# Performance work log

Hardware: AMD Instinct MI355X
Metric: run time of the kernel (lower is better)

## Reference

```python
import jax, jax.numpy as jnp
import numpy as np

NUM_HEAD = 16
D_Q = 512
D_KV = 512
ROPE_BASE = 10000.0


def _cos_sin(seq_len, dim):
    # Replicates calculate_cos_sin: theta = base**(-2*ids) / (dim//2)
    pos = jnp.arange(seq_len, dtype=jnp.float32)[:, None]          # (S,1)
    ids = jnp.arange(dim // 2, dtype=jnp.float32)                  # (D/2,)
    theta = (ROPE_BASE ** (-2.0 * ids)) / (dim // 2)
    r = pos * theta[None, :]                                       # (S, D/2)
    return jnp.cos(r), jnp.sin(r)


def _rope(x, cos, sin):
    b, s, d = x.shape
    xv = x.reshape(b, s, d // 2, 2)
    x0, x1 = xv[..., 0], xv[..., 1]
    out = jnp.stack([x0 * cos - x1 * sin, x1 * cos + x0 * sin], axis=-1)
    return out.reshape(b, s, d)


def setup_inputs() -> dict:
    key = jax.random.key(0)
    ks = jax.random.split(key, 10)
    d_model, d_q, d_kv = 1024, D_Q, D_KV
    b, s = 2, 2048
    w = lambda k, i, o: jax.random.normal(k, (i, o), dtype=jnp.float32) * 0.02
    return {
        "x": jax.random.normal(ks[0], (b, s, d_model), dtype=jnp.float32),
        "Wd_q_w": w(ks[1], d_model, d_q), "Wd_q_b": jnp.zeros((d_q,), jnp.float32),
        "Wu_q_w": w(ks[2], d_q, d_model), "Wu_q_b": jnp.zeros((d_model,), jnp.float32),
        "Wq_r_w": w(ks[3], d_q, d_model), "Wq_r_b": jnp.zeros((d_model,), jnp.float32),
        "Wk_r_w": w(ks[4], d_model, d_model), "Wk_r_b": jnp.zeros((d_model,), jnp.float32),
        "Wd_kv_w": w(ks[5], d_model, d_kv), "Wd_kv_b": jnp.zeros((d_kv,), jnp.float32),
        "Wu_k_w": w(ks[6], d_kv, d_model), "Wu_k_b": jnp.zeros((d_model,), jnp.float32),
        "Wu_v_w": w(ks[7], d_kv, d_model), "Wu_v_b": jnp.zeros((d_model,), jnp.float32),
        "Wo_w": w(ks[8], d_model, d_model), "Wo_b": jnp.zeros((d_model,), jnp.float32),
    }


def reference(x, Wd_q_w, Wd_q_b, Wu_q_w, Wu_q_b, Wq_r_w, Wq_r_b,
              Wk_r_w, Wk_r_b, Wd_kv_w, Wd_kv_b, Wu_k_w, Wu_k_b,
              Wu_v_w, Wu_v_b, Wo_w, Wo_b):
    b, s, d_model = x.shape
    h = NUM_HEAD
    hd = d_model // h
    scale = jnp.sqrt(jnp.float32(h + D_KV + D_Q))

    def heads(t):  # (b,s,d) -> (b,h,s,hd)
        return t.reshape(b, s, h, hd).transpose(0, 2, 1, 3)

    cos, sin = _cos_sin(s, d_model)

    ct_q = x @ Wd_q_w + Wd_q_b                                   # (b,s,d_q)
    qt_c = heads(ct_q @ Wu_q_w + Wu_q_b)
    qt_r = heads(_rope(ct_q @ Wq_r_w + Wq_r_b, cos, sin))
    query = qt_c + qt_r                                          # (b,h,s,hd)

    ct_kv = x @ Wd_kv_w + Wd_kv_b                                # (b,s,d_kv)
    kt_c = heads(ct_kv @ Wu_k_w + Wu_k_b)
    kt_r = heads(_rope(x @ Wk_r_w + Wk_r_b, cos, sin))
    key = kt_c + kt_r
    value = heads(ct_kv @ Wu_v_w + Wu_v_b)

    attn = jnp.einsum('bhqd,bhkd->bhqk', query, key) / scale
    attn = jax.nn.softmax(attn, axis=-1)
    out = jnp.einsum('bhqk,bhkd->bhqd', attn, value)
    out = out.transpose(0, 2, 1, 3).reshape(b, s, d_model)
    return out @ Wo_w + Wo_b
```

## Files before the change

kernel.cpp:

```cpp
#include <hip/hip_runtime.h>
#include <hip/hip_bf16.h>
#include <math.h>
#include <limits.h>

typedef __hip_bfloat16 bf16;
typedef __bf16 bf16x8 __attribute__((ext_vector_type(8)));
typedef float  f32x4  __attribute__((ext_vector_type(4)));

#define DEVI __device__ __forceinline__

static constexpr int Bb     = 2;
static constexpr int Ss     = 2048;
static constexpr int DMODEL = 1024;
static constexpr int NTOK   = Bb * Ss;

DEVI float bf2f(bf16 v) { return __bfloat162float(v); }
DEVI bf16  f2bf(float v) { return __float2bfloat16(v); }

DEVI unsigned int packbf(float lo, float hi) {
  union { bf16 b; unsigned short u; } a, c;
  a.b = f2bf(lo); c.b = f2bf(hi);
  return ((unsigned int)c.u << 16) | a.u;
}
DEVI float bfu2f(unsigned short u) {
  unsigned int x = (unsigned int)u << 16;
  float f; __builtin_memcpy(&f, &x, 4); return f;
}

DEVI void async_load16(const bf16* g, bf16* l) {
  __builtin_amdgcn_global_load_lds((const __attribute__((address_space(1))) void*)g,
                                   (__attribute__((address_space(3))) void*)l, 16, 0, 0);
}

__global__ __launch_bounds__(256) void convert_kernel(
    const float* __restrict__ in, bf16* __restrict__ out, int n4) {
  const int t = blockIdx.x * blockDim.x + threadIdx.x;
  if (t >= n4) return;
  const float4 v = ((const float4*)in)[t];
  uint2 o; o.x = packbf(v.x, v.y); o.y = packbf(v.z, v.w);
  *(uint2*)&out[(size_t)t * 4] = o;
}

struct TransDesc { const float* src; bf16* dst; int R; int C; int tstart; };
struct TransPack { TransDesc d[8]; };

__global__ __launch_bounds__(256) void transpose8_kernel(TransPack p) {
  const int t = blockIdx.x;
  int i = 0;
#pragma unroll
  for (int j = 1; j < 8; ++j) if (t >= p.d[j].tstart) i = j;
  const float* __restrict__ in = p.d[i].src;
  bf16* __restrict__ out = p.d[i].dst;
  const int R = p.d[i].R, C = p.d[i].C;
  const int rel = t - p.d[i].tstart;
  const int tilesC = C >> 6;
  const int r0 = (rel / tilesC) * 64, c0 = (rel % tilesC) * 64;

  __shared__ bf16 tl[64][65];
  const int tc = threadIdx.x & 63, tr = threadIdx.x >> 6;
#pragma unroll
  for (int q = 0; q < 16; ++q) {
    int r = tr + q * 4;
    tl[r][tc] = f2bf(in[(size_t)(r0 + r) * C + c0 + tc]);
  }
  __syncthreads();
#pragma unroll
  for (int q = 0; q < 16; ++q) {
    int r = tr + q * 4;
    out[(size_t)(c0 + r) * R + r0 + tc] = tl[tc][r];
  }
}

struct GemmDesc {
  const bf16* A; const bf16* WT; const float* b1; const float* b2; bf16* C;
  int lda, ldb, ldc, K, bsplit, nTX, blkStart, biasRow;
};
struct GemmBatch { GemmDesc d[4]; };

__global__ __launch_bounds__(256) void gemm_batch_kernel(GemmBatch gb) {
  const int t = blockIdx.x;
  int di = 0;
#pragma unroll
  for (int j = 1; j < 4; ++j) if (t >= gb.d[j].blkStart) di = j;
  const GemmDesc D = gb.d[di];
  const int rel = t - D.blkStart;
  const int tileN = (rel % D.nTX) * 128;
  const int tileM = (rel / D.nTX) * 128;

  __shared__ bf16 ldsA[128 * 32];
  __shared__ bf16 ldsB[128 * 32];
  const int tid = threadIdx.x;
  const int lane = tid & 63;
  const int w = tid >> 6;
  const int wr = w >> 1, wc = w & 1;
  const int l15 = lane & 15, lg = lane >> 4;
  const int lrow = lane >> 2;
  const int lcol = (lane & 3) * 8;

  f32x4 acc[4][4] = {};

  for (int k0 = 0; k0 < D.K; k0 += 32) {
    async_load16(D.A  + (size_t)(tileM + w * 32 +      lrow) * D.lda + k0 + lcol, &ldsA[(w * 32) * 32]);
    async_load16(D.A  + (size_t)(tileM + w * 32 + 16 + lrow) * D.lda + k0 + lcol, &ldsA[(w * 32 + 16) * 32]);
    async_load16(D.WT + (size_t)(tileN + w * 32 +      lrow) * D.ldb + k0 + lcol, &ldsB[(w * 32) * 32]);
    async_load16(D.WT + (size_t)(tileN + w * 32 + 16 + lrow) * D.ldb + k0 + lcol, &ldsB[(w * 32 + 16) * 32]);
    __syncthreads();

    bf16x8 af[4], bfr[4];
#pragma unroll
    for (int i = 0; i < 4; ++i) {
      af[i]  = *(const bf16x8*)&ldsA[(wr * 64 + i * 16 + l15) * 32 + lg * 8];
      bfr[i] = *(const bf16x8*)&ldsB[(wc * 64 + i * 16 + l15) * 32 + lg * 8];
    }
#pragma unroll
    for (int i = 0; i < 4; ++i)
#pragma unroll
      for (int j = 0; j < 4; ++j)
        acc[i][j] = __builtin_amdgcn_mfma_f32_16x16x32_bf16(af[i], bfr[j], acc[i][j], 0, 0, 0);
    __syncthreads();
  }

  const int mbase = tileM + wr * 64;
  const int nbase = tileN + wc * 64;
#pragma unroll
  for (int j = 0; j < 4; ++j) {
    int col = nbase + j * 16 + l15;
    float bvc = D.biasRow ? 0.0f : (col < D.bsplit ? D.b1[col] : D.b2[col - D.bsplit]);
#pragma unroll
    for (int i = 0; i < 4; ++i)
#pragma unroll
      for (int r = 0; r < 4; ++r) {
        int row = mbase + i * 16 + lg * 4 + r;
        float bv = D.biasRow ? D.b1[row] : bvc;
        D.C[(size_t)row * D.ldc + col] = f2bf(acc[i][j][r] + bv);
      }
  }
}

__global__ __launch_bounds__(256) void gemm_kernel_f32(
    const bf16* __restrict__ A, int lda,
    const bf16* __restrict__ WT, int ldb,
    const float* __restrict__ b1,
    float* __restrict__ Cout, int ldc, int K) {
  __shared__ bf16 ldsA[128 * 32];
  __shared__ bf16 ldsB[128 * 32];
  const int tid = threadIdx.x;
  const int lane = tid & 63;
  const int w = tid >> 6;
  const int wr = w >> 1, wc = w & 1;
  const int tileM = blockIdx.y * 128;
  const int tileN = blockIdx.x * 128;
  const int l15 = lane & 15, lg = lane >> 4;
  const int lrow = lane >> 2;
  const int lcol = (lane & 3) * 8;

  f32x4 acc[4][4] = {};

  for (int k0 = 0; k0 < K; k0 += 32) {
    async_load16(A  + (size_t)(tileM + w * 32 +      lrow) * lda + k0 + lcol, &ldsA[(w * 32) * 32]);
    async_load16(A  + (size_t)(tileM + w * 32 + 16 + lrow) * lda + k0 + lcol, &ldsA[(w * 32 + 16) * 32]);
    async_load16(WT + (size_t)(tileN + w * 32 +      lrow) * ldb + k0 + lcol, &ldsB[(w * 32) * 32]);
    async_load16(WT + (size_t)(tileN + w * 32 + 16 + lrow) * ldb + k0 + lcol, &ldsB[(w * 32 + 16) * 32]);
    __syncthreads();

    bf16x8 af[4], bfr[4];
#pragma unroll
    for (int i = 0; i < 4; ++i) {
      af[i]  = *(const bf16x8*)&ldsA[(wr * 64 + i * 16 + l15) * 32 + lg * 8];
      bfr[i] = *(const bf16x8*)&ldsB[(wc * 64 + i * 16 + l15) * 32 + lg * 8];
    }
#pragma unroll
    for (int i = 0; i < 4; ++i)
#pragma unroll
      for (int j = 0; j < 4; ++j)
        acc[i][j] = __builtin_amdgcn_mfma_f32_16x16x32_bf16(af[i], bfr[j], acc[i][j], 0, 0, 0);
    __syncthreads();
  }

  const int mbase = tileM + wr * 64;
  const int nbase = tileN + wc * 64;
#pragma unroll
  for (int j = 0; j < 4; ++j) {
    int col = nbase + j * 16 + l15;
    float bvc = b1[col];
#pragma unroll
    for (int i = 0; i < 4; ++i)
#pragma unroll
      for (int r = 0; r < 4; ++r) {
        int row = mbase + i * 16 + lg * 4 + r;
        Cout[(size_t)row * ldc + col] = acc[i][j][r] + bvc;
      }
  }
}

__global__ __launch_bounds__(256) void combine_rope_kernel(
    const bf16* __restrict__ Gc, int ldc_,
    const bf16* __restrict__ Gr, int ldr_,
    bf16* __restrict__ out) {
  const int t = blockIdx.x * blockDim.x + threadIdx.x;
  const int g = t & 127, row = t >> 7;
  const int s = row & (Ss - 1);
  union { bf16x8 v; unsigned short u[8]; } vc, vr;
  vc.v = *(const bf16x8*)&Gc[(size_t)row * ldc_ + (size_t)g * 8];
  vr.v = *(const bf16x8*)&Gr[(size_t)row * ldr_ + (size_t)g * 8];
  uint4 o;
  unsigned int* op = &o.x;
#pragma unroll
  for (int qq = 0; qq < 4; ++qq) {
    const int p = g * 4 + qq;
    float c, sn;
    if (p == 0) {
      float rr = (float)s * (1.0f / 512.0f);
      c = cosf(rr); sn = sinf(rr);
    } else {
      float theta = exp2f(-26.5754247590989f * (float)p) * (1.0f / 512.0f);
      sn = (float)s * theta; c = 1.0f;
    }
    float g0 = bfu2f(vr.u[2 * qq]), g1 = bfu2f(vr.u[2 * qq + 1]);
    float c0 = bfu2f(vc.u[2 * qq]), c1 = bfu2f(vc.u[2 * qq + 1]);
    op[qq] = packbf(c0 + g0 * c - g1 * sn, c1 + g1 * c + g0 * sn);
  }
  *(uint4*)&out[(size_t)row * DMODEL + (size_t)g * 8] = o;
}

__global__ __launch_bounds__(256) void attn_kernel(
    const bf16* __restrict__ Qn, const bf16* __restrict__ Kn,
    const bf16* __restrict__ VT, bf16* __restrict__ AO) {
  const int bh = blockIdx.x, qt = blockIdx.y;
  const int b = bh >> 4, h = bh & 15;
  const int tid = threadIdx.x, lane = tid & 63, w = tid >> 6;
  const int q0 = qt * 64 + w * 16;
  const int l15 = lane & 15, lg = lane >> 4;
  const float SC2 = 0.044736075f;
  const float THR = 11.5415603f;

  __shared__ bf16 ldsK[2][64 * 64];
  __shared__ bf16 ldsV[2][64 * 64];
  __shared__ bf16 ldsP[4][16 * 64];

  const bf16* Kg = Kn + (size_t)(b * Ss) * DMODEL + h * 64;
  const bf16* Vg = VT + (size_t)(h * 64) * NTOK + b * Ss;

  const int r0 = tid >> 3;
  const int srcb = ((tid & 7) * 16) ^ ((r0 & 7) << 4);
  const char* kS0 = (const char*)(Kg + (size_t)r0 * DMODEL) + srcb;
  const char* kS1 = (const char*)(Kg + (size_t)(32 + r0) * DMODEL) + srcb;
  const char* vS0 = (const char*)(Vg + (size_t)r0 * NTOK) + srcb;
  const char* vS1 = (const char*)(Vg + (size_t)(32 + r0) * NTOK) + srcb;
  const ptrdiff_t kAdv = (ptrdiff_t)64 * DMODEL * 2;
  const ptrdiff_t vAdv = 128;

  bf16* kd0_b0 = &ldsK[0][w * 512]; bf16* kd1_b0 = &ldsK[0][2048 + w * 512];
  bf16* kd0_b1 = &ldsK[1][w * 512]; bf16* kd1_b1 = &ldsK[1][2048 + w * 512];
  bf16* vd0_b0 = &ldsV[0][w * 512]; bf16* vd1_b0 = &ldsV[0][2048 + w * 512];
  bf16* vd0_b1 = &ldsV[1][w * 512]; bf16* vd1_b1 = &ldsV[1][2048 + w * 512];

  auto stageTo = [&](bf16* kd0, bf16* kd1, bf16* vd0, bf16* vd1) {
    async_load16((const bf16*)kS0, kd0);
    async_load16((const bf16*)kS1, kd1);
    async_load16((const bf16*)vS0, vd0);
    async_load16((const bf16*)vS1, vd1);
    kS0 += kAdv; kS1 += kAdv; vS0 += vAdv; vS1 += vAdv;
  };

  const int kswz = (l15 & 7) << 4;
  const int xA = (lg * 16) ^ kswz;
  const int xB = (64 + lg * 16) ^ kswz;
  const char* krA0 = (const char*)&ldsK[0][0] + l15 * 128 + xA;
  const char* krB0 = (const char*)&ldsK[0][0] + l15 * 128 + xB;
  const char* krA1 = (const char*)&ldsK[1][0] + l15 * 128 + xA;
  const char* krB1 = (const char*)&ldsK[1][0] + l15 * 128 + xB;
  const char* vrA0 = (const char*)&ldsV[0][0] + l15 * 128 + xA;
  const char* vrB0 = (const char*)&ldsV[0][0] + l15 * 128 + xB;
  const char* vrA1 = (const char*)&ldsV[1][0] + l15 * 128 + xA;
  const char* vrB1 = (const char*)&ldsV[1][0] + l15 * 128 + xB;

  char* Pw = (char*)&ldsP[w][0];
  char* pwr[4];
#pragma unroll
  for (int j = 0; j < 4; ++j) {
    const int chunk = (j * 2 + (lg >> 1)) ^ (l15 & 7);
    pwr[j] = Pw + l15 * 128 + chunk * 16 + (lg & 1) * 8;
  }
  const char* paA = Pw + l15 * 128 + xA;
  const char* paB = Pw + l15 * 128 + xB;

  const bf16* Qbase = Qn + (size_t)(b * Ss + q0 + l15) * DMODEL + h * 64;
  bf16x8 bq0 = *(const bf16x8*)&Qbase[lg * 8];
  bf16x8 bq1 = *(const bf16x8*)&Qbase[32 + lg * 8];

  float m = 0.0f, l = 0.0f;
  f32x4 accO[4] = {};

  auto body = [&](const char* krA, const char* krB, const char* vrA, const char* vrB) {
    f32x4 sa[4] = {};
#pragma unroll
    for (int j = 0; j < 4; ++j) {
      bf16x8 ak0 = *(const bf16x8*)(krA + j * 2048);
      bf16x8 ak1 = *(const bf16x8*)(krB + j * 2048);
      sa[j] = __builtin_amdgcn_mfma_f32_16x16x32_bf16(ak0, bq0, sa[j], 0, 0, 0);
      sa[j] = __builtin_amdgcn_mfma_f32_16x16x32_bf16(ak1, bq1, sa[j], 0, 0, 0);
    }
    float pmaxr = -3.0e38f;
#pragma unroll
    for (int j = 0; j < 4; ++j)
#pragma unroll
      for (int r = 0; r < 4; ++r) pmaxr = fmaxf(pmaxr, sa[j][r]);
    if (__any(fmaf(pmaxr, SC2, -m) > THR)) {
      float px = fmaxf(pmaxr, __shfl_xor(pmaxr, 16, 64));
      px = fmaxf(px, __shfl_xor(px, 32, 64));
      float mnew = fmaxf(m, px * SC2);
      float corr = __builtin_amdgcn_exp2f(m - mnew);
      m = mnew; l *= corr;
      float cr[4];
#pragma unroll
      for (int r = 0; r < 4; ++r) cr[r] = __shfl(corr, lg * 4 + r, 64);
#pragma unroll
      for (int dj = 0; dj < 4; ++dj)
#pragma unroll
        for (int r = 0; r < 4; ++r) accO[dj][r] *= cr[r];
    }
    float p[4][4];
    float ts0 = 0.f, ts1 = 0.f;
#pragma unroll
    for (int j = 0; j < 4; ++j) {
#pragma unroll
      for (int r = 0; r < 4; ++r)
        p[j][r] = __builtin_amdgcn_exp2f(fmaf(sa[j][r], SC2, -m));
      ts0 += p[j][0] + p[j][2];
      ts1 += p[j][1] + p[j][3];
    }
    float ts = ts0 + ts1;
    ts += __shfl_xor(ts, 16, 64);
    ts += __shfl_xor(ts, 32, 64);
    l += ts;
#pragma unroll
    for (int j = 0; j < 4; ++j) {
      uint2 pw;
      pw.x = packbf(p[j][0], p[j][1]);
      pw.y = packbf(p[j][2], p[j][3]);
      *(uint2*)pwr[j] = pw;
    }
    bf16x8 pa0 = *(const bf16x8*)paA;
    bf16x8 pa1 = *(const bf16x8*)paB;
#pragma unroll
    for (int dj = 0; dj < 4; ++dj) {
      bf16x8 bv0 = *(const bf16x8*)(vrA + dj * 2048);
      bf16x8 bv1 = *(const bf16x8*)(vrB + dj * 2048);
      accO[dj] = __builtin_amdgcn_mfma_f32_16x16x32_bf16(pa0, bv0, accO[dj], 0, 0, 0);
      accO[dj] = __builtin_amdgcn_mfma_f32_16x16x32_bf16(pa1, bv1, accO[dj], 0, 0, 0);
    }
  };

  stageTo(kd0_b0, kd1_b0, vd0_b0, vd1_b0);
  for (int tt = 0; tt < 16; ++tt) {
    __syncthreads();
    stageTo(kd0_b1, kd1_b1, vd0_b1, vd1_b1);
    body(krA0, krB0, vrA0, vrB0);
    __syncthreads();
    if (tt < 15) stageTo(kd0_b0, kd1_b0, vd0_b0, vd1_b0);
    body(krA1, krB1, vrA1, vrB1);
  }

  float linv[4];
#pragma unroll
  for (int r = 0; r < 4; ++r) linv[r] = 1.0f / __shfl(l, lg * 4 + r, 64);
#pragma unroll
  for (int dj = 0; dj < 4; ++dj)
#pragma unroll
    for (int r = 0; r < 4; ++r)
      AO[(size_t)(b * Ss + q0 + lg * 4 + r) * DMODEL + h * 64 + dj * 16 + l15] =
          f2bf(accO[dj][r] * linv[r]);
}

extern "C" void kernel_launch(void* const* d_in, const int* in_sizes, int n_in,
                              void* d_out, int out_size, void* d_ws, size_t ws_size,
                              hipStream_t stream) {
  const float* x      = (const float*)d_in[0];
  const float* Wdq    = (const float*)d_in[1];  const float* Wdq_b  = (const float*)d_in[2];
  const float* Wuq    = (const float*)d_in[3];  const float* Wuq_b  = (const float*)d_in[4];
  const float* Wqr    = (const float*)d_in[5];  const float* Wqr_b  = (const float*)d_in[6];
  const float* Wkr    = (const float*)d_in[7];  const float* Wkr_b  = (const float*)d_in[8];
  const float* Wdkv   = (const float*)d_in[9];  const float* Wdkv_b = (const float*)d_in[10];
  const float* Wuk    = (const float*)d_in[11]; const float* Wuk_b  = (const float*)d_in[12];
  const float* Wuv    = (const float*)d_in[13]; const float* Wuv_b  = (const float*)d_in[14];
  const float* Wo     = (const float*)d_in[15]; const float* Wo_b   = (const float*)d_in[16];

  char* ws = (char*)d_ws;
  size_t off = 0;
  bf16* WdqT   = (bf16*)(ws + off); off += (size_t)512  * 1024 * 2;
  bf16* WdkvT  = (bf16*)(ws + off); off += (size_t)512  * 1024 * 2;
  bf16* WuqT   = (bf16*)(ws + off); off += (size_t)1024 * 512  * 2;
  bf16* WqrT   = (bf16*)(ws + off); off += (size_t)1024 * 512  * 2;
  bf16* WukT   = (bf16*)(ws + off); off += (size_t)1024 * 512  * 2;
  bf16* WuvT   = (bf16*)(ws + off); off += (size_t)1024 * 512  * 2;
  bf16* WkrT   = (bf16*)(ws + off); off += (size_t)1024 * 1024 * 2;
  bf16* WoT    = (bf16*)(ws + off); off += (size_t)1024 * 1024 * 2;
  bf16* x_bf   = (bf16*)(ws + off); off += (size_t)NTOK * 1024 * 2;
  bf16* ct     = (bf16*)(ws + off); off += (size_t)NTOK * 1024 * 2;
  bf16* Ga     = (bf16*)(ws + off); off += (size_t)NTOK * 1024 * 2;
  bf16* VTr    = (bf16*)(ws + off); off += (size_t)NTOK * 1024 * 2;
  bf16* Gupk   = x_bf;
  bf16* Qn     = (bf16*)d_out;
  bf16* Kn     = (bf16*)d_out + (size_t)NTOK * DMODEL;
  bf16* AO     = Ga;
  (void)ws_size; (void)in_sizes; (void)n_in; (void)out_size;

  TransPack tp = {{
    { Wdq,  WdqT,  1024, 512,  0    },
    { Wdkv, WdkvT, 1024, 512,  128  },
    { Wuq,  WuqT,  512,  1024, 256  },
    { Wqr,  WqrT,  512,  1024, 384  },
    { Wuk,  WukT,  512,  1024, 512  },
    { Wuv,  WuvT,  512,  1024, 640  },
    { Wkr,  WkrT,  1024, 1024, 768  },
    { Wo,   WoT,   1024, 1024, 1024 },
  }};
  transpose8_kernel<<<1280, 256, 0, stream>>>(tp);
  convert_kernel<<<(NTOK * DMODEL / 4 + 255) / 256, 256, 0, stream>>>(x, x_bf, NTOK * DMODEL / 4);

  GemmBatch ba = {{
    { x_bf, WdqT, Wdq_b, Wdkv_b, ct, 1024, 1024, 1024, 1024, 512,     8, 0,       0 },
    { x_bf, WkrT, Wkr_b, Wkr_b,  Kn, 1024, 1024, 1024, 1024, INT_MAX, 8, 256,     0 },
    { 0, 0, 0, 0, 0, 0, 0, 0, 0, 0, 1, INT_MAX, 0 },
    { 0, 0, 0, 0, 0, 0, 0, 0, 0, 0, 1, INT_MAX, 0 },
  }};
  gemm_batch_kernel<<<512, 256, 0, stream>>>(ba);

  GemmBatch bb = {{
    { ct,       WuqT,     Wuq_b, Wuq_b, Ga,   1024, 512,  1024, 512, INT_MAX, 8,  0,   0 },
    { ct,       WqrT,     Wqr_b, Wqr_b, Qn,   1024, 512,  1024, 512, INT_MAX, 8,  256, 0 },
    { ct + 512, WukT,     Wuk_b, Wuk_b, Gupk, 1024, 512,  1024, 512, INT_MAX, 8,  512, 0 },
    { WuvT,     ct + 512, Wuv_b, Wuv_b, VTr,  512,  1024, NTOK, 512, INT_MAX, 32, 768, 1 },
  }};
  gemm_batch_kernel<<<1024, 256, 0, stream>>>(bb);

  combine_rope_kernel<<<NTOK * 128 / 256, 256, 0, stream>>>(Ga, 1024, Qn, 1024, Qn);
  combine_rope_kernel<<<NTOK * 128 / 256, 256, 0, stream>>>(Gupk, 1024, Kn, 1024, Kn);

  attn_kernel<<<dim3(32, 32), 256, 0, stream>>>(Qn, Kn, VTr, AO);

  gemm_kernel_f32<<<dim3(8, 32), 256, 0, stream>>>(
      AO, 1024, WoT, 1024, Wo_b, (float*)d_out, 1024, 1024);
}
```

Baseline: 197.4 us.

## Fuse weight transpose with input conversion, retile output GEMM, prioritize attention MFMAs

```diff
diff --git a/kernel.cpp b/kernel.cpp
--- a/kernel.cpp
+++ b/kernel.cpp
@@ -32,20 +32,20 @@
                                    (__attribute__((address_space(3))) void*)l, 16, 0, 0);
 }
 
-__global__ __launch_bounds__(256) void convert_kernel(
-    const float* __restrict__ in, bf16* __restrict__ out, int n4) {
-  const int t = blockIdx.x * blockDim.x + threadIdx.x;
-  if (t >= n4) return;
-  const float4 v = ((const float4*)in)[t];
-  uint2 o; o.x = packbf(v.x, v.y); o.y = packbf(v.z, v.w);
-  *(uint2*)&out[(size_t)t * 4] = o;
-}
-
 struct TransDesc { const float* src; bf16* dst; int R; int C; int tstart; };
 struct TransPack { TransDesc d[8]; };
 
-__global__ __launch_bounds__(256) void transpose8_kernel(TransPack p) {
+__global__ __launch_bounds__(256) void trans_conv_kernel(
+    TransPack p, const float* __restrict__ cx, bf16* __restrict__ cxo, int tstartConv) {
+  __shared__ bf16 tl[64][65];
   const int t = blockIdx.x;
+  if (t >= tstartConv) {
+    const int idx = (t - tstartConv) * 256 + threadIdx.x;
+    const float4 v = ((const float4*)cx)[idx];
+    uint2 o; o.x = packbf(v.x, v.y); o.y = packbf(v.z, v.w);
+    *(uint2*)&cxo[(size_t)idx * 4] = o;
+    return;
+  }
   int i = 0;
 #pragma unroll
   for (int j = 1; j < 8; ++j) if (t >= p.d[j].tstart) i = j;
@@ -55,8 +55,6 @@
   const int rel = t - p.d[i].tstart;
   const int tilesC = C >> 6;
   const int r0 = (rel / tilesC) * 64, c0 = (rel % tilesC) * 64;
-
-  __shared__ bf16 tl[64][65];
   const int tc = threadIdx.x & 63, tr = threadIdx.x >> 6;
 #pragma unroll
   for (int q = 0; q < 16; ++q) {
@@ -143,51 +141,48 @@
     const float* __restrict__ b1,
     float* __restrict__ Cout, int ldc, int K) {
   __shared__ bf16 ldsA[128 * 32];
-  __shared__ bf16 ldsB[128 * 32];
+  __shared__ bf16 ldsB[64 * 32];
   const int tid = threadIdx.x;
   const int lane = tid & 63;
   const int w = tid >> 6;
-  const int wr = w >> 1, wc = w & 1;
   const int tileM = blockIdx.y * 128;
-  const int tileN = blockIdx.x * 128;
+  const int tileN = blockIdx.x * 64;
   const int l15 = lane & 15, lg = lane >> 4;
   const int lrow = lane >> 2;
   const int lcol = (lane & 3) * 8;
 
-  f32x4 acc[4][4] = {};
+  f32x4 acc[2][4] = {};
 
   for (int k0 = 0; k0 < K; k0 += 32) {
     async_load16(A  + (size_t)(tileM + w * 32 +      lrow) * lda + k0 + lcol, &ldsA[(w * 32) * 32]);
     async_load16(A  + (size_t)(tileM + w * 32 + 16 + lrow) * lda + k0 + lcol, &ldsA[(w * 32 + 16) * 32]);
-    async_load16(WT + (size_t)(tileN + w * 32 +      lrow) * ldb + k0 + lcol, &ldsB[(w * 32) * 32]);
-    async_load16(WT + (size_t)(tileN + w * 32 + 16 + lrow) * ldb + k0 + lcol, &ldsB[(w * 32 + 16) * 32]);
-    __syncthreads();
-
-    bf16x8 af[4], bfr[4];
-#pragma unroll
-    for (int i = 0; i < 4; ++i) {
-      af[i]  = *(const bf16x8*)&ldsA[(wr * 64 + i * 16 + l15) * 32 + lg * 8];
-      bfr[i] = *(const bf16x8*)&ldsB[(wc * 64 + i * 16 + l15) * 32 + lg * 8];
-    }
-#pragma unroll
-    for (int i = 0; i < 4; ++i)
+    async_load16(WT + (size_t)(tileN + w * 16 + lrow) * ldb + k0 + lcol, &ldsB[(w * 16) * 32]);
+    __syncthreads();
+
+    bf16x8 af[2], bfr[4];
+#pragma unroll
+    for (int i = 0; i < 2; ++i)
+      af[i]  = *(const bf16x8*)&ldsA[(w * 32 + i * 16 + l15) * 32 + lg * 8];
+#pragma unroll
+    for (int j = 0; j < 4; ++j)
+      bfr[j] = *(const bf16x8*)&ldsB[(j * 16 + l15) * 32 + lg * 8];
+#pragma unroll
+    for (int i = 0; i < 2; ++i)
 #pragma unroll
       for (int j = 0; j < 4; ++j)
         acc[i][j] = __builtin_amdgcn_mfma_f32_16x16x32_bf16(af[i], bfr[j], acc[i][j], 0, 0, 0);
     __syncthreads();
   }
 
-  const int mbase = tileM + wr * 64;
-  const int nbase = tileN + wc * 64;
 #pragma unroll
   for (int j = 0; j < 4; ++j) {
-    int col = nbase + j * 16 + l15;
+    int col = tileN + j * 16 + l15;
     float bvc = b1[col];
 #pragma unroll
-    for (int i = 0; i < 4; ++i)
+    for (int i = 0; i < 2; ++i)
 #pragma unroll
       for (int r = 0; r < 4; ++r) {
-        int row = mbase + i * 16 + lg * 4 + r;
+        int row = tileM + w * 32 + i * 16 + lg * 4 + r;
         Cout[(size_t)row * ldc + col] = acc[i][j][r] + bvc;
       }
   }
@@ -294,6 +289,7 @@
 
   auto body = [&](const char* krA, const char* krB, const char* vrA, const char* vrB) {
     f32x4 sa[4] = {};
+    __builtin_amdgcn_s_setprio(1);
 #pragma unroll
     for (int j = 0; j < 4; ++j) {
       bf16x8 ak0 = *(const bf16x8*)(krA + j * 2048);
@@ -301,6 +297,7 @@
       sa[j] = __builtin_amdgcn_mfma_f32_16x16x32_bf16(ak0, bq0, sa[j], 0, 0, 0);
       sa[j] = __builtin_amdgcn_mfma_f32_16x16x32_bf16(ak1, bq1, sa[j], 0, 0, 0);
     }
+    __builtin_amdgcn_s_setprio(0);
     float pmaxr = -3.0e38f;
 #pragma unroll
     for (int j = 0; j < 4; ++j)
@@ -343,6 +340,7 @@
     }
     bf16x8 pa0 = *(const bf16x8*)paA;
     bf16x8 pa1 = *(const bf16x8*)paB;
+    __builtin_amdgcn_s_setprio(1);
 #pragma unroll
     for (int dj = 0; dj < 4; ++dj) {
       bf16x8 bv0 = *(const bf16x8*)(vrA + dj * 2048);
@@ -350,6 +348,7 @@
       accO[dj] = __builtin_amdgcn_mfma_f32_16x16x32_bf16(pa0, bv0, accO[dj], 0, 0, 0);
       accO[dj] = __builtin_amdgcn_mfma_f32_16x16x32_bf16(pa1, bv1, accO[dj], 0, 0, 0);
     }
+    __builtin_amdgcn_s_setprio(0);
   };
 
   stageTo(kd0_b0, kd1_b0, vd0_b0, vd1_b0);
@@ -416,8 +415,7 @@
     { Wkr,  WkrT,  1024, 1024, 768  },
     { Wo,   WoT,   1024, 1024, 1024 },
   }};
-  transpose8_kernel<<<1280, 256, 0, stream>>>(tp);
-  convert_kernel<<<(NTOK * DMODEL / 4 + 255) / 256, 256, 0, stream>>>(x, x_bf, NTOK * DMODEL / 4);
+  trans_conv_kernel<<<1280 + 4096, 256, 0, stream>>>(tp, x, x_bf, 1280);
 
   GemmBatch ba = {{
     { x_bf, WdqT, Wdq_b, Wdkv_b, ct, 1024, 1024, 1024, 1024, 512,     8, 0,       0 },
@@ -440,6 +438,6 @@
 
   attn_kernel<<<dim3(32, 32), 256, 0, stream>>>(Qn, Kn, VTr, AO);
 
-  gemm_kernel_f32<<<dim3(8, 32), 256, 0, stream>>>(
+  gemm_kernel_f32<<<dim3(16, 32), 256, 0, stream>>>(
       AO, 1024, WoT, 1024, Wo_b, (float*)d_out, 1024, 1024);
 }
```

Measured after the change: 189.6 us. 1.04x faster.
